# Performance work log

Measured on AMD Instinct MI355X. Metric: run time of the kernel, lower is better.

## Reference

```python
import math
import jax, jax.numpy as jnp
import numpy as np


def _sinkhorn_attn(q, n):
    """Log-domain Sinkhorn-Knopp, eps=1, max_iter=1, uniform marginals.
    cost C = -q @ q^T, so M = (-C + u + v)/eps = S + u + v with S = q q^T.
    Returns transport plan pi = exp(S + u_i + v_j).  q: [B, n, d]."""
    S = jnp.einsum('bnd,bmd->bnm', q, q)            # [B, n, n]
    log_marg = -math.log(n)                          # log(1/n)
    u = log_marg - jax.nn.logsumexp(S, axis=-1)      # [B, n] row update
    v = log_marg - jax.nn.logsumexp(S + u[..., :, None], axis=-2)  # [B, n] col update
    return jnp.exp(S + u[..., :, None] + v[..., None, :])


def reference(x, row_embed, col_embed):
    # x: [B, d, H, W]; row_embed/col_embed: [len_embedding, d//2]
    B, d, H, W = x.shape
    # learned positional embedding: [H, W, d] -> [d, H, W]
    x_emb = col_embed[:W]                             # [W, F]
    y_emb = row_embed[:H]                             # [H, F]
    F = x_emb.shape[-1]
    pos = jnp.concatenate([
        jnp.broadcast_to(x_emb[None, :, :], (H, W, F)),
        jnp.broadcast_to(y_emb[:, None, :], (H, W, F)),
    ], axis=-1).transpose(2, 0, 1)                    # [d, H, W]
    x = x + pos[None]

    n = H * W
    xf = x.reshape(B, d, n).transpose(0, 2, 1)        # [B, n, d] = q = k = v (v unscaled)
    inv_sqrtV = 1.0 / math.sqrt(math.sqrt(d))         # d**-0.25 applied to q and k each
    attn = _sinkhorn_attn(xf * inv_sqrtV, n)          # [B, n, n]
    out = jnp.einsum('bnm,bmd->bnd', attn, xf)        # [B, n, d]
    return out.transpose(0, 2, 1).reshape(B, d, H, W)


def setup_inputs() -> dict:
    key = jax.random.key(0)
    k1, k2, k3 = jax.random.split(key, 3)
    B, d, H, W = 32, 512, 32, 32
    len_emb, F = 32, d // 2
    return {
        'x': jax.random.normal(k1, (B, d, H, W), dtype=jnp.float32),
        'row_embed': jax.random.uniform(k2, (len_emb, F), dtype=jnp.float32),
        'col_embed': jax.random.uniform(k3, (len_emb, F), dtype=jnp.float32),
    }
```

## Files before the change

kernel.cpp:

```cpp
#include <hip/hip_runtime.h>
#include <hip/hip_fp16.h>
#include <math.h>

typedef _Float16 f16;
typedef _Float16 f16x8 __attribute__((ext_vector_type(8)));
typedef _Float16 f16x4 __attribute__((ext_vector_type(4)));
typedef float f32x4 __attribute__((ext_vector_type(4)));

namespace {
constexpr int kB = 32, kD = 512, kN = 1024, kF = 256;
constexpr float kScale = 0.04419417382415922f;
constexpr float kLogMarg = -6.931471805599453f;
constexpr float kMarg = 1.f / 1024.f;
constexpr float kPScale = 16384.f;
constexpr float kPInv = 1.f / 16384.f;
}

__device__ __forceinline__ void gload16(const void* g, void* l) {
  __builtin_amdgcn_global_load_lds(
      (const __attribute__((address_space(1))) void*)g,
      (__attribute__((address_space(3))) void*)l, 16, 0, 0);
}

__global__ __launch_bounds__(256) void k_prep(
    const float* __restrict__ x, const float* __restrict__ re,
    const float* __restrict__ ce, f16* __restrict__ xf,
    f16* __restrict__ xfT, int b0) {
  __shared__ f16 T[64][68];
  const int lb = blockIdx.z;
  const int i0 = blockIdx.x * 64, c0 = blockIdx.y * 64;
  const int t = threadIdx.x;
  const int il = (t & 15) * 4;
  const int cl = t >> 4;
  const size_t xbase = ((size_t)(b0 + lb) * kD) * kN;
#pragma unroll
  for (int p = 0; p < 4; p++) {
    const int c = c0 + cl + 16 * p;
    const int i = i0 + il;
    const float4 xv = *(const float4*)(x + xbase + (size_t)c * kN + i);
    float4 pv;
    if (c < kF) {
      pv.x = ce[((i + 0) & 31) * kF + c];
      pv.y = ce[((i + 1) & 31) * kF + c];
      pv.z = ce[((i + 2) & 31) * kF + c];
      pv.w = ce[((i + 3) & 31) * kF + c];
    } else {
      const float r = re[(i >> 5) * kF + (c - kF)];
      pv.x = r; pv.y = r; pv.z = r; pv.w = r;
    }
    const f16 h0 = (f16)(xv.x + pv.x), h1 = (f16)(xv.y + pv.y);
    const f16 h2 = (f16)(xv.z + pv.z), h3 = (f16)(xv.w + pv.w);
    f16* dT = xfT + ((size_t)lb * kD + c) * kN + i;
    *(f16x4*)dT = (f16x4){h0, h1, h2, h3};
    T[cl + 16 * p][il + 0] = h0; T[cl + 16 * p][il + 1] = h1;
    T[cl + 16 * p][il + 2] = h2; T[cl + 16 * p][il + 3] = h3;
  }
  __syncthreads();
#pragma unroll
  for (int p = 0; p < 4; p++) {
    const int ir = cl + 16 * p;
    const int cc = il;
    const f16 h0 = T[cc + 0][ir], h1 = T[cc + 1][ir];
    const f16 h2 = T[cc + 2][ir], h3 = T[cc + 3][ir];
    f16* dF = xf + ((size_t)lb * kN + i0 + ir) * kD + c0 + cc;
    *(f16x4*)dF = (f16x4){h0, h1, h2, h3};
  }
}

__global__ __launch_bounds__(256) void k_gemm_s(
    const f16* __restrict__ xf, f16* __restrict__ S16,
    float* __restrict__ rp) {
  __shared__ char sm[65536];
  const int nwg = (int)(gridDim.x * gridDim.y * gridDim.z);
  const int lin = (int)(blockIdx.x +
                        gridDim.x * (blockIdx.y + gridDim.y * blockIdx.z));
  const int wid = (lin & 7) * (nwg >> 3) + (lin >> 3);
  const int bx = wid & 7, by = (wid >> 3) & 7, bz = wid >> 6;

  const int lb = bz;
  const int i0 = by * 128, j0 = bx * 128;
  const char* base = (const char*)(xf + (size_t)lb * kN * kD);
  const int t = threadIdx.x;
  const int w = t >> 6, lane = t & 63;
  const int m_off = (w >> 1) * 64, n_off = (w & 1) * 64;
  const int quad = lane >> 4, l15 = lane & 15;
  const int swz = (l15 & 7) << 4;

  int srcA[4], srcB[4], ldsw[4];
#pragma unroll
  for (int p = 0; p < 4; p++) {
    const int off = p * 4096 + w * 1024 + lane * 16;
    const int r = off >> 7;
    const int cb = (off & 127) ^ ((r & 7) << 4);
    srcA[p] = (i0 + r) * (kD * 2) + cb;
    srcB[p] = (j0 + r) * (kD * 2) + cb;
    ldsw[p] = p * 4096 + w * 1024;
  }

  f32x4 acc[4][4];
#pragma unroll
  for (int a = 0; a < 4; a++)
#pragma unroll
    for (int b = 0; b < 4; b++) acc[a][b] = (f32x4){0.f, 0.f, 0.f, 0.f};

#pragma unroll
  for (int p = 0; p < 4; p++) gload16(base + srcA[p], sm + ldsw[p]);
#pragma unroll
  for (int p = 0; p < 4; p++) gload16(base + srcB[p], sm + 16384 + ldsw[p]);
  __syncthreads();

#pragma unroll
  for (int tt = 0; tt < 8; tt++) {
    const int cur = tt & 1, nxt = cur ^ 1;
    if (tt + 1 < 8) {
      const int k0b = (tt + 1) * 128;
#pragma unroll
      for (int p = 0; p < 4; p++)
        gload16(base + srcA[p] + k0b, sm + (nxt << 15) + ldsw[p]);
#pragma unroll
      for (int p = 0; p < 4; p++)
        gload16(base + srcB[p] + k0b, sm + (nxt << 15) + 16384 + ldsw[p]);
    }
    const char* bA = sm + (cur << 15);
    const char* bB = bA + 16384;
#pragma unroll
    for (int kk = 0; kk < 2; kk++) {
      f16x8 af[4], bf[4];
#pragma unroll
      for (int q = 0; q < 4; q++)
        af[q] = *(const f16x8*)(bA + (m_off + 16 * q + l15) * 128 +
                                ((kk * 64 + quad * 16) ^ swz));
#pragma unroll
      for (int q = 0; q < 4; q++)
        bf[q] = *(const f16x8*)(bB + (n_off + 16 * q + l15) * 128 +
                                ((kk * 64 + quad * 16) ^ swz));
#pragma unroll
      for (int qa = 0; qa < 4; qa++)
#pragma unroll
        for (int qb = 0; qb < 4; qb++)
          acc[qa][qb] = __builtin_amdgcn_mfma_f32_16x16x32_f16(
              af[qa], bf[qb], acc[qa][qb], 0, 0, 0);
    }
    __syncthreads();
  }

  f16* Sb = S16 + (size_t)lb * kN * kN;
  const int jt2 = bx * 2 + (w & 1);
  float* rpb = rp + ((size_t)lb * 16 + jt2) * kN + i0 + m_off;
#pragma unroll
  for (int qa = 0; qa < 4; qa++) {
    const int i = i0 + m_off + 16 * qa + quad * 4;
    float rs[4] = {0.f, 0.f, 0.f, 0.f};
#pragma unroll
    for (int qb = 0; qb < 4; qb++) {
      const int j = j0 + n_off + 16 * qb + l15;
#pragma unroll
      for (int r = 0; r < 4; r++) {
        const f16 h = (f16)(acc[qa][qb][r] * kScale);
        Sb[(size_t)(i + r) * kN + j] = h;
        rs[r] += __expf((float)h);
      }
    }
#pragma unroll
    for (int r = 0; r < 4; r++) {
      float s = rs[r];
      s += __shfl_xor(s, 1);
      s += __shfl_xor(s, 2);
      s += __shfl_xor(s, 4);
      s += __shfl_xor(s, 8);
      if (l15 == 0) rpb[16 * qa + 4 * quad + r] = s;
    }
  }
}

__global__ __launch_bounds__(256) void k_u(
    const float* __restrict__ rp, float* __restrict__ u) {
  const int lb = blockIdx.y;
  const int i = blockIdx.x * 256 + threadIdx.x;
  const float* r = rp + (size_t)lb * 16 * kN + i;
  float s = 0.f;
#pragma unroll
  for (int t = 0; t < 16; t++) s += r[(size_t)t * kN];
  u[lb * kN + i] = kLogMarg - __logf(s);
}

__global__ __launch_bounds__(256) void k_cs(
    const f16* __restrict__ S16, const float* __restrict__ u,
    float* __restrict__ cp) {
  const int lb = blockIdx.z;
  const int seg = blockIdx.y;
  const int j = blockIdx.x * 256 + threadIdx.x;
  const f16* Sb = S16 + (size_t)lb * kN * kN + j;
  const float* ub = u + lb * kN + seg * 64;
  const size_t rbase = (size_t)(seg * 64) * kN;
  float s = 0.f;
#pragma unroll 4
  for (int r = 0; r < 64; r++)
    s += __expf((float)Sb[rbase + (size_t)r * kN] + ub[r]);
  cp[((size_t)lb * 16 + seg) * kN + j] = s;
}

__global__ __launch_bounds__(256) void k_v(
    const float* __restrict__ cp, float* __restrict__ ev) {
  const int lb = blockIdx.y;
  const int j = blockIdx.x * 256 + threadIdx.x;
  const float* c = cp + (size_t)lb * 16 * kN + j;
  float s = 0.f;
#pragma unroll
  for (int r = 0; r < 16; r++) s += c[(size_t)r * kN];
  ev[lb * kN + j] = kMarg / s;
}

__global__ __launch_bounds__(256) void k_pt(
    const f16* __restrict__ S16, const float* __restrict__ u,
    const float* __restrict__ ev, f16* __restrict__ t16) {
  const int row = blockIdx.x;
  const float ui = u[row];
  const f16* Sr = S16 + (size_t)row * kN;
  const float* evb = ev + (size_t)(row >> 10) * kN;
  f16* Tr = t16 + (size_t)row * kN;
  const int j = threadIdx.x * 4;
  const f16x4 s = *(const f16x4*)(Sr + j);
  const float4 e = *(const float4*)(evb + j);
  f16x4 o;
  o[0] = (f16)(__expf((float)s[0] + ui) * e.x * kPScale);
  o[1] = (f16)(__expf((float)s[1] + ui) * e.y * kPScale);
  o[2] = (f16)(__expf((float)s[2] + ui) * e.z * kPScale);
  o[3] = (f16)(__expf((float)s[3] + ui) * e.w * kPScale);
  *(f16x4*)(Tr + j) = o;
}

__global__ __launch_bounds__(256) void k_gemm_o(
    const f16* __restrict__ xfT, const f16* __restrict__ P,
    float* __restrict__ out, int b0) {
  __shared__ char sm[65536];
  const int nwg = (int)(gridDim.x * gridDim.y * gridDim.z);
  const int lin = (int)(blockIdx.x +
                        gridDim.x * (blockIdx.y + gridDim.y * blockIdx.z));
  const int wid = (lin & 7) * (nwg >> 3) + (lin >> 3);
  const int bx = wid & 7, by = (wid >> 3) & 3, bz = wid >> 5;

  const int lb = bz;
  const int i0 = bx * 128, c0 = by * 128;
  const char* Ab = (const char*)(xfT + (size_t)lb * kD * kN);
  const char* Bb = (const char*)(P + (size_t)lb * kN * kN);
  const int t = threadIdx.x;
  const int w = t >> 6, lane = t & 63;
  const int m_off = (w >> 1) * 64, n_off = (w & 1) * 64;
  const int quad = lane >> 4, l15 = lane & 15;
  const int swz = (l15 & 7) << 4;

  int srcA[4], srcB[4], ldsw[4];
#pragma unroll
  for (int p = 0; p < 4; p++) {
    const int off = p * 4096 + w * 1024 + lane * 16;
    const int r = off >> 7;
    const int cb = (off & 127) ^ ((r & 7) << 4);
    srcA[p] = (c0 + r) * (kN * 2) + cb;
    srcB[p] = (i0 + r) * (kN * 2) + cb;
    ldsw[p] = p * 4096 + w * 1024;
  }

  f32x4 acc[4][4];
#pragma unroll
  for (int a = 0; a < 4; a++)
#pragma unroll
    for (int b = 0; b < 4; b++) acc[a][b] = (f32x4){0.f, 0.f, 0.f, 0.f};

#pragma unroll
  for (int p = 0; p < 4; p++) gload16(Ab + srcA[p], sm + ldsw[p]);
#pragma unroll
  for (int p = 0; p < 4; p++) gload16(Bb + srcB[p], sm + 16384 + ldsw[p]);
  __syncthreads();

#pragma unroll
  for (int tt = 0; tt < 16; tt++) {
    const int cur = tt & 1, nxt = cur ^ 1;
    if (tt + 1 < 16) {
      const int k0b = (tt + 1) * 128;
#pragma unroll
      for (int p = 0; p < 4; p++)
        gload16(Ab + srcA[p] + k0b, sm + (nxt << 15) + ldsw[p]);
#pragma unroll
      for (int p = 0; p < 4; p++)
        gload16(Bb + srcB[p] + k0b, sm + (nxt << 15) + 16384 + ldsw[p]);
    }
    const char* bA = sm + (cur << 15);
    const char* bB = bA + 16384;
#pragma unroll
    for (int kk = 0; kk < 2; kk++) {
      f16x8 af[4], bf[4];
#pragma unroll
      for (int q = 0; q < 4; q++)
        af[q] = *(const f16x8*)(bA + (m_off + 16 * q + l15) * 128 +
                                ((kk * 64 + quad * 16) ^ swz));
#pragma unroll
      for (int q = 0; q < 4; q++)
        bf[q] = *(const f16x8*)(bB + (n_off + 16 * q + l15) * 128 +
                                ((kk * 64 + quad * 16) ^ swz));
#pragma unroll
      for (int qa = 0; qa < 4; qa++)
#pragma unroll
        for (int qb = 0; qb < 4; qb++)
          acc[qa][qb] = __builtin_amdgcn_mfma_f32_16x16x32_f16(
              af[qa], bf[qb], acc[qa][qb], 0, 0, 0);
    }
    __syncthreads();
  }

  float* ob = out + ((size_t)(b0 + lb) * kD) * kN;
#pragma unroll
  for (int qa = 0; qa < 4; qa++) {
    const int c = c0 + m_off + 16 * qa + quad * 4;
#pragma unroll
    for (int qb = 0; qb < 4; qb++) {
      const int i = i0 + n_off + 16 * qb + l15;
#pragma unroll
      for (int r = 0; r < 4; r++)
        ob[(size_t)(c + r) * kN + i] = acc[qa][qb][r] * kPInv;
    }
  }
}

extern "C" void kernel_launch(void* const* d_in, const int* in_sizes, int n_in,
                              void* d_out, int out_size, void* d_ws, size_t ws_size,
                              hipStream_t stream) {
  const float* x = (const float*)d_in[0];
  const float* re = (const float*)d_in[1];
  const float* ce = (const float*)d_in[2];
  float* out = (float*)d_out;

  char* wsb = (char*)d_ws;
  const size_t perb = 2097152ull + 1048576 + 1048576 + 2097152 +
                      4096 + 4096 + 65536 + 65536;
  int G = (int)(ws_size / perb);
  if (G >= 32) G = 32;
  else if (G >= 16) G = 16;
  else if (G >= 8) G = 8;
  else if (G >= 4) G = 4;
  else if (G < 1) G = 1;
  f16* S16 = (f16*)wsb;
  f16* xf = (f16*)(wsb + (size_t)G * 2097152);
  f16* xfT = (f16*)((char*)xf + (size_t)G * 1048576);
  f16* t16 = (f16*)((char*)xfT + (size_t)G * 1048576);
  float* u = (float*)((char*)t16 + (size_t)G * 2097152);
  float* ev = u + (size_t)G * kN;
  float* rp = ev + (size_t)G * kN;
  float* cp = rp + (size_t)G * 16 * kN;

  for (int b0 = 0; b0 < kB; b0 += G) {
    const int g = (kB - b0 < G) ? (kB - b0) : G;
    k_prep<<<dim3(16, 8, g), 256, 0, stream>>>(x, re, ce, xf, xfT, b0);
    k_gemm_s<<<dim3(8, 8, g), 256, 0, stream>>>(xf, S16, rp);
    k_u<<<dim3(4, g), 256, 0, stream>>>(rp, u);
    k_cs<<<dim3(4, 16, g), 256, 0, stream>>>(S16, u, cp);
    k_v<<<dim3(4, g), 256, 0, stream>>>(cp, ev);
    k_pt<<<g * kN, 256, 0, stream>>>(S16, u, ev, t16);
    k_gemm_o<<<dim3(8, 4, g), 256, 0, stream>>>(xfT, t16, out, b0);
  }
}
```

Measured before the change: 256.1 us.

## Fuse exp-plan materialization into column-sum pass and fold column scaling into output GEMM

```diff
diff --git a/kernel.cpp b/kernel.cpp
--- a/kernel.cpp
+++ b/kernel.cpp
@@ -67,46 +67,47 @@
   }
 }
 
-__global__ __launch_bounds__(256) void k_gemm_s(
+__global__ __launch_bounds__(512) void k_gemm_s(
     const f16* __restrict__ xf, f16* __restrict__ S16,
     float* __restrict__ rp) {
-  __shared__ char sm[65536];
+  __shared__ char sm[131072];
   const int nwg = (int)(gridDim.x * gridDim.y * gridDim.z);
   const int lin = (int)(blockIdx.x +
                         gridDim.x * (blockIdx.y + gridDim.y * blockIdx.z));
   const int wid = (lin & 7) * (nwg >> 3) + (lin >> 3);
-  const int bx = wid & 7, by = (wid >> 3) & 7, bz = wid >> 6;
+  const int bx = wid & 3, by = (wid >> 2) & 3, bz = wid >> 4;
 
   const int lb = bz;
-  const int i0 = by * 128, j0 = bx * 128;
+  const int i0 = by * 256, j0 = bx * 256;
   const char* base = (const char*)(xf + (size_t)lb * kN * kD);
   const int t = threadIdx.x;
   const int w = t >> 6, lane = t & 63;
-  const int m_off = (w >> 1) * 64, n_off = (w & 1) * 64;
+  const int wm = w >> 2, wn = w & 3;
+  const int m_off = wm * 128, n_off = wn * 64;
   const int quad = lane >> 4, l15 = lane & 15;
   const int swz = (l15 & 7) << 4;
 
   int srcA[4], srcB[4], ldsw[4];
 #pragma unroll
   for (int p = 0; p < 4; p++) {
-    const int off = p * 4096 + w * 1024 + lane * 16;
+    const int off = p * 8192 + t * 16;
     const int r = off >> 7;
     const int cb = (off & 127) ^ ((r & 7) << 4);
     srcA[p] = (i0 + r) * (kD * 2) + cb;
     srcB[p] = (j0 + r) * (kD * 2) + cb;
-    ldsw[p] = p * 4096 + w * 1024;
-  }
-
-  f32x4 acc[4][4];
-#pragma unroll
-  for (int a = 0; a < 4; a++)
+    ldsw[p] = p * 8192 + w * 1024;
+  }
+
+  f32x4 acc[8][4];
+#pragma unroll
+  for (int a = 0; a < 8; a++)
 #pragma unroll
     for (int b = 0; b < 4; b++) acc[a][b] = (f32x4){0.f, 0.f, 0.f, 0.f};
 
 #pragma unroll
   for (int p = 0; p < 4; p++) gload16(base + srcA[p], sm + ldsw[p]);
 #pragma unroll
-  for (int p = 0; p < 4; p++) gload16(base + srcB[p], sm + 16384 + ldsw[p]);
+  for (int p = 0; p < 4; p++) gload16(base + srcB[p], sm + 32768 + ldsw[p]);
   __syncthreads();
 
 #pragma unroll
@@ -116,18 +117,18 @@
       const int k0b = (tt + 1) * 128;
 #pragma unroll
       for (int p = 0; p < 4; p++)
-        gload16(base + srcA[p] + k0b, sm + (nxt << 15) + ldsw[p]);
+        gload16(base + srcA[p] + k0b, sm + (nxt << 16) + ldsw[p]);
 #pragma unroll
       for (int p = 0; p < 4; p++)
-        gload16(base + srcB[p] + k0b, sm + (nxt << 15) + 16384 + ldsw[p]);
-    }
-    const char* bA = sm + (cur << 15);
-    const char* bB = bA + 16384;
+        gload16(base + srcB[p] + k0b, sm + (nxt << 16) + 32768 + ldsw[p]);
+    }
+    const char* bA = sm + (cur << 16);
+    const char* bB = bA + 32768;
 #pragma unroll
     for (int kk = 0; kk < 2; kk++) {
-      f16x8 af[4], bf[4];
-#pragma unroll
-      for (int q = 0; q < 4; q++)
+      f16x8 af[8], bf[4];
+#pragma unroll
+      for (int q = 0; q < 8; q++)
         af[q] = *(const f16x8*)(bA + (m_off + 16 * q + l15) * 128 +
                                 ((kk * 64 + quad * 16) ^ swz));
 #pragma unroll
@@ -135,7 +136,7 @@
         bf[q] = *(const f16x8*)(bB + (n_off + 16 * q + l15) * 128 +
                                 ((kk * 64 + quad * 16) ^ swz));
 #pragma unroll
-      for (int qa = 0; qa < 4; qa++)
+      for (int qa = 0; qa < 8; qa++)
 #pragma unroll
         for (int qb = 0; qb < 4; qb++)
           acc[qa][qb] = __builtin_amdgcn_mfma_f32_16x16x32_f16(
@@ -145,10 +146,10 @@
   }
 
   f16* Sb = S16 + (size_t)lb * kN * kN;
-  const int jt2 = bx * 2 + (w & 1);
-  float* rpb = rp + ((size_t)lb * 16 + jt2) * kN + i0 + m_off;
-#pragma unroll
-  for (int qa = 0; qa < 4; qa++) {
+  const int jt = bx * 4 + wn;
+  float* rpb = rp + ((size_t)lb * 16 + jt) * kN + i0 + m_off;
+#pragma unroll
+  for (int qa = 0; qa < 8; qa++) {
     const int i = i0 + m_off + 16 * qa + quad * 4;
     float rs[4] = {0.f, 0.f, 0.f, 0.f};
 #pragma unroll
@@ -186,17 +187,21 @@
 
 __global__ __launch_bounds__(256) void k_cs(
     const f16* __restrict__ S16, const float* __restrict__ u,
-    float* __restrict__ cp) {
+    float* __restrict__ cp, f16* __restrict__ E16) {
   const int lb = blockIdx.z;
   const int seg = blockIdx.y;
   const int j = blockIdx.x * 256 + threadIdx.x;
   const f16* Sb = S16 + (size_t)lb * kN * kN + j;
+  f16* Eb = E16 + (size_t)lb * kN * kN + j;
   const float* ub = u + lb * kN + seg * 64;
   const size_t rbase = (size_t)(seg * 64) * kN;
   float s = 0.f;
 #pragma unroll 4
-  for (int r = 0; r < 64; r++)
-    s += __expf((float)Sb[rbase + (size_t)r * kN] + ub[r]);
+  for (int r = 0; r < 64; r++) {
+    const float eS = __expf((float)Sb[rbase + (size_t)r * kN] + ub[r]);
+    s += eS;
+    Eb[rbase + (size_t)r * kN] = (f16)(eS * kPScale);
+  }
   cp[((size_t)lb * 16 + seg) * kN + j] = s;
 }
 
@@ -211,87 +216,97 @@
   ev[lb * kN + j] = kMarg / s;
 }
 
-__global__ __launch_bounds__(256) void k_pt(
-    const f16* __restrict__ S16, const float* __restrict__ u,
-    const float* __restrict__ ev, f16* __restrict__ t16) {
-  const int row = blockIdx.x;
-  const float ui = u[row];
-  const f16* Sr = S16 + (size_t)row * kN;
-  const float* evb = ev + (size_t)(row >> 10) * kN;
-  f16* Tr = t16 + (size_t)row * kN;
-  const int j = threadIdx.x * 4;
-  const f16x4 s = *(const f16x4*)(Sr + j);
-  const float4 e = *(const float4*)(evb + j);
-  f16x4 o;
-  o[0] = (f16)(__expf((float)s[0] + ui) * e.x * kPScale);
-  o[1] = (f16)(__expf((float)s[1] + ui) * e.y * kPScale);
-  o[2] = (f16)(__expf((float)s[2] + ui) * e.z * kPScale);
-  o[3] = (f16)(__expf((float)s[3] + ui) * e.w * kPScale);
-  *(f16x4*)(Tr + j) = o;
-}
-
-__global__ __launch_bounds__(256) void k_gemm_o(
-    const f16* __restrict__ xfT, const f16* __restrict__ P,
-    float* __restrict__ out, int b0) {
-  __shared__ char sm[65536];
+__global__ __launch_bounds__(512) void k_gemm_o(
+    const f16* __restrict__ xfT, const f16* __restrict__ E16,
+    const float* __restrict__ ev, float* __restrict__ out, int b0) {
+  __shared__ char sm[131072];
   const int nwg = (int)(gridDim.x * gridDim.y * gridDim.z);
   const int lin = (int)(blockIdx.x +
                         gridDim.x * (blockIdx.y + gridDim.y * blockIdx.z));
   const int wid = (lin & 7) * (nwg >> 3) + (lin >> 3);
-  const int bx = wid & 7, by = (wid >> 3) & 3, bz = wid >> 5;
+  const int bx = wid & 3, by = (wid >> 2) & 1, bz = wid >> 3;
 
   const int lb = bz;
-  const int i0 = bx * 128, c0 = by * 128;
+  const int i0 = bx * 256, c0 = by * 256;
   const char* Ab = (const char*)(xfT + (size_t)lb * kD * kN);
-  const char* Bb = (const char*)(P + (size_t)lb * kN * kN);
+  const char* Bb = (const char*)(E16 + (size_t)lb * kN * kN);
+  const float* evb = ev + (size_t)lb * kN;
   const int t = threadIdx.x;
   const int w = t >> 6, lane = t & 63;
-  const int m_off = (w >> 1) * 64, n_off = (w & 1) * 64;
+  const int wm = w >> 2, wn = w & 3;
+  const int m_off = wm * 128, n_off = wn * 64;
   const int quad = lane >> 4, l15 = lane & 15;
   const int swz = (l15 & 7) << 4;
 
-  int srcA[4], srcB[4], ldsw[4];
-#pragma unroll
-  for (int p = 0; p < 4; p++) {
-    const int off = p * 4096 + w * 1024 + lane * 16;
+  int srcAlin[4], dstA[4], srcB[4], ldsw[4], evcol[4];
+#pragma unroll
+  for (int p = 0; p < 4; p++) {
+    const int off = p * 8192 + t * 16;
     const int r = off >> 7;
-    const int cb = (off & 127) ^ ((r & 7) << 4);
-    srcA[p] = (c0 + r) * (kN * 2) + cb;
+    const int cbl = off & 127;
+    const int cb = cbl ^ ((r & 7) << 4);
+    srcAlin[p] = (c0 + r) * (kN * 2) + cbl;
+    dstA[p] = r * 128 + cb;
     srcB[p] = (i0 + r) * (kN * 2) + cb;
-    ldsw[p] = p * 4096 + w * 1024;
-  }
-
-  f32x4 acc[4][4];
-#pragma unroll
-  for (int a = 0; a < 4; a++)
+    ldsw[p] = p * 8192 + w * 1024;
+    evcol[p] = cbl >> 1;
+  }
+
+  f32x4 acc[8][4];
+#pragma unroll
+  for (int a = 0; a < 8; a++)
 #pragma unroll
     for (int b = 0; b < 4; b++) acc[a][b] = (f32x4){0.f, 0.f, 0.f, 0.f};
 
-#pragma unroll
-  for (int p = 0; p < 4; p++) gload16(Ab + srcA[p], sm + ldsw[p]);
-#pragma unroll
-  for (int p = 0; p < 4; p++) gload16(Bb + srcB[p], sm + 16384 + ldsw[p]);
+  f16x8 al[4];
+  float4 e0[4], e1[4];
+#pragma unroll
+  for (int p = 0; p < 4; p++) {
+    al[p] = *(const f16x8*)(Ab + srcAlin[p]);
+    e0[p] = *(const float4*)(evb + evcol[p]);
+    e1[p] = *(const float4*)(evb + evcol[p] + 4);
+  }
+#pragma unroll
+  for (int p = 0; p < 4; p++) gload16(Bb + srcB[p], sm + 32768 + ldsw[p]);
+#pragma unroll
+  for (int p = 0; p < 4; p++) {
+    f16x8 pr;
+    pr[0] = (f16)((float)al[p][0] * e0[p].x);
+    pr[1] = (f16)((float)al[p][1] * e0[p].y);
+    pr[2] = (f16)((float)al[p][2] * e0[p].z);
+    pr[3] = (f16)((float)al[p][3] * e0[p].w);
+    pr[4] = (f16)((float)al[p][4] * e1[p].x);
+    pr[5] = (f16)((float)al[p][5] * e1[p].y);
+    pr[6] = (f16)((float)al[p][6] * e1[p].z);
+    pr[7] = (f16)((float)al[p][7] * e1[p].w);
+    *(f16x8*)(sm + dstA[p]) = pr;
+  }
   __syncthreads();
 
 #pragma unroll
   for (int tt = 0; tt < 16; tt++) {
     const int cur = tt & 1, nxt = cur ^ 1;
-    if (tt + 1 < 16) {
+    const bool pf = (tt + 1 < 16);
+    if (pf) {
       const int k0b = (tt + 1) * 128;
+      const int k0f = (tt + 1) * 64;
+#pragma unroll
+      for (int p = 0; p < 4; p++) {
+        al[p] = *(const f16x8*)(Ab + srcAlin[p] + k0b);
+        e0[p] = *(const float4*)(evb + k0f + evcol[p]);
+        e1[p] = *(const float4*)(evb + k0f + evcol[p] + 4);
+      }
 #pragma unroll
       for (int p = 0; p < 4; p++)
-        gload16(Ab + srcA[p] + k0b, sm + (nxt << 15) + ldsw[p]);
-#pragma unroll
-      for (int p = 0; p < 4; p++)
-        gload16(Bb + srcB[p] + k0b, sm + (nxt << 15) + 16384 + ldsw[p]);
-    }
-    const char* bA = sm + (cur << 15);
-    const char* bB = bA + 16384;
+        gload16(Bb + srcB[p] + k0b, sm + (nxt << 16) + 32768 + ldsw[p]);
+    }
+    const char* bA = sm + (cur << 16);
+    const char* bB = bA + 32768;
 #pragma unroll
     for (int kk = 0; kk < 2; kk++) {
-      f16x8 af[4], bf[4];
-#pragma unroll
-      for (int q = 0; q < 4; q++)
+      f16x8 af[8], bf[4];
+#pragma unroll
+      for (int q = 0; q < 8; q++)
         af[q] = *(const f16x8*)(bA + (m_off + 16 * q + l15) * 128 +
                                 ((kk * 64 + quad * 16) ^ swz));
 #pragma unroll
@@ -299,18 +314,33 @@
         bf[q] = *(const f16x8*)(bB + (n_off + 16 * q + l15) * 128 +
                                 ((kk * 64 + quad * 16) ^ swz));
 #pragma unroll
-      for (int qa = 0; qa < 4; qa++)
+      for (int qa = 0; qa < 8; qa++)
 #pragma unroll
         for (int qb = 0; qb < 4; qb++)
           acc[qa][qb] = __builtin_amdgcn_mfma_f32_16x16x32_f16(
               af[qa], bf[qb], acc[qa][qb], 0, 0, 0);
     }
+    if (pf) {
+#pragma unroll
+      for (int p = 0; p < 4; p++) {
+        f16x8 pr;
+        pr[0] = (f16)((float)al[p][0] * e0[p].x);
+        pr[1] = (f16)((float)al[p][1] * e0[p].y);
+        pr[2] = (f16)((float)al[p][2] * e0[p].z);
+        pr[3] = (f16)((float)al[p][3] * e0[p].w);
+        pr[4] = (f16)((float)al[p][4] * e1[p].x);
+        pr[5] = (f16)((float)al[p][5] * e1[p].y);
+        pr[6] = (f16)((float)al[p][6] * e1[p].z);
+        pr[7] = (f16)((float)al[p][7] * e1[p].w);
+        *(f16x8*)(sm + (nxt << 16) + dstA[p]) = pr;
+      }
+    }
     __syncthreads();
   }
 
   float* ob = out + ((size_t)(b0 + lb) * kD) * kN;
 #pragma unroll
-  for (int qa = 0; qa < 4; qa++) {
+  for (int qa = 0; qa < 8; qa++) {
     const int c = c0 + m_off + 16 * qa + quad * 4;
 #pragma unroll
     for (int qb = 0; qb < 4; qb++) {
@@ -342,8 +372,8 @@
   f16* S16 = (f16*)wsb;
   f16* xf = (f16*)(wsb + (size_t)G * 2097152);
   f16* xfT = (f16*)((char*)xf + (size_t)G * 1048576);
-  f16* t16 = (f16*)((char*)xfT + (size_t)G * 1048576);
-  float* u = (float*)((char*)t16 + (size_t)G * 2097152);
+  f16* E16 = (f16*)((char*)xfT + (size_t)G * 1048576);
+  float* u = (float*)((char*)E16 + (size_t)G * 2097152);
   float* ev = u + (size_t)G * kN;
   float* rp = ev + (size_t)G * kN;
   float* cp = rp + (size_t)G * 16 * kN;
@@ -351,11 +381,10 @@
   for (int b0 = 0; b0 < kB; b0 += G) {
     const int g = (kB - b0 < G) ? (kB - b0) : G;
     k_prep<<<dim3(16, 8, g), 256, 0, stream>>>(x, re, ce, xf, xfT, b0);
-    k_gemm_s<<<dim3(8, 8, g), 256, 0, stream>>>(xf, S16, rp);
+    k_gemm_s<<<dim3(4, 4, g), 512, 0, stream>>>(xf, S16, rp);
     k_u<<<dim3(4, g), 256, 0, stream>>>(rp, u);
-    k_cs<<<dim3(4, 16, g), 256, 0, stream>>>(S16, u, cp);
+    k_cs<<<dim3(4, 16, g), 256, 0, stream>>>(S16, u, cp, E16);
     k_v<<<dim3(4, g), 256, 0, stream>>>(cp, ev);
-    k_pt<<<g * kN, 256, 0, stream>>>(S16, u, ev, t16);
-    k_gemm_o<<<dim3(8, 4, g), 256, 0, stream>>>(xfT, t16, out, b0);
-  }
-}
+    k_gemm_o<<<dim3(4, 2, g), 512, 0, stream>>>(xfT, E16, ev, out, b0);
+  }
+}
```

After: 257.0 us. No clear change (+0.3%).

## Fuse transport-plan exponentiation into output GEMM with larger tiles and staged pipeline

Applied to the files above, without the earlier changes.

```diff
diff --git a/kernel.cpp b/kernel.cpp
--- a/kernel.cpp
+++ b/kernel.cpp
@@ -11,8 +11,6 @@
 constexpr int kB = 32, kD = 512, kN = 1024, kF = 256;
 constexpr float kScale = 0.04419417382415922f;
 constexpr float kLogMarg = -6.931471805599453f;
-constexpr float kMarg = 1.f / 1024.f;
-constexpr float kPScale = 16384.f;
 constexpr float kPInv = 1.f / 16384.f;
 }
 
@@ -189,128 +187,192 @@
     float* __restrict__ cp) {
   const int lb = blockIdx.z;
   const int seg = blockIdx.y;
-  const int j = blockIdx.x * 256 + threadIdx.x;
-  const f16* Sb = S16 + (size_t)lb * kN * kN + j;
+  const int j = threadIdx.x * 4;
+  const f16* Sb = S16 + (size_t)lb * kN * kN + (size_t)(seg * 64) * kN + j;
   const float* ub = u + lb * kN + seg * 64;
-  const size_t rbase = (size_t)(seg * 64) * kN;
-  float s = 0.f;
-#pragma unroll 4
-  for (int r = 0; r < 64; r++)
-    s += __expf((float)Sb[rbase + (size_t)r * kN] + ub[r]);
-  cp[((size_t)lb * 16 + seg) * kN + j] = s;
+  float s0 = 0.f, s1 = 0.f, s2 = 0.f, s3 = 0.f;
+#pragma unroll 8
+  for (int r = 0; r < 64; r++) {
+    const f16x4 v = *(const f16x4*)(Sb + (size_t)r * kN);
+    const float ur = ub[r];
+    s0 += __expf((float)v[0] + ur);
+    s1 += __expf((float)v[1] + ur);
+    s2 += __expf((float)v[2] + ur);
+    s3 += __expf((float)v[3] + ur);
+  }
+  float4 o = {s0, s1, s2, s3};
+  *(float4*)(cp + ((size_t)lb * 16 + seg) * kN + j) = o;
 }
 
 __global__ __launch_bounds__(256) void k_v(
-    const float* __restrict__ cp, float* __restrict__ ev) {
+    const float* __restrict__ cp, float* __restrict__ evp) {
   const int lb = blockIdx.y;
   const int j = blockIdx.x * 256 + threadIdx.x;
   const float* c = cp + (size_t)lb * 16 * kN + j;
   float s = 0.f;
 #pragma unroll
   for (int r = 0; r < 16; r++) s += c[(size_t)r * kN];
-  ev[lb * kN + j] = kMarg / s;
-}
-
-__global__ __launch_bounds__(256) void k_pt(
-    const f16* __restrict__ S16, const float* __restrict__ u,
-    const float* __restrict__ ev, f16* __restrict__ t16) {
-  const int row = blockIdx.x;
-  const float ui = u[row];
-  const f16* Sr = S16 + (size_t)row * kN;
-  const float* evb = ev + (size_t)(row >> 10) * kN;
-  f16* Tr = t16 + (size_t)row * kN;
-  const int j = threadIdx.x * 4;
-  const f16x4 s = *(const f16x4*)(Sr + j);
-  const float4 e = *(const float4*)(evb + j);
-  f16x4 o;
-  o[0] = (f16)(__expf((float)s[0] + ui) * e.x * kPScale);
-  o[1] = (f16)(__expf((float)s[1] + ui) * e.y * kPScale);
-  o[2] = (f16)(__expf((float)s[2] + ui) * e.z * kPScale);
-  o[3] = (f16)(__expf((float)s[3] + ui) * e.w * kPScale);
-  *(f16x4*)(Tr + j) = o;
-}
-
-__global__ __launch_bounds__(256) void k_gemm_o(
-    const f16* __restrict__ xfT, const f16* __restrict__ P,
+  evp[lb * kN + j] = 16.f / s;
+}
+
+#define AF_READ(q)                                                          \
+  _Pragma("unroll")                                                         \
+  for (int pa = 0; pa < 2; pa++)                                            \
+    _Pragma("unroll")                                                       \
+    for (int kk = 0; kk < 2; kk++)                                          \
+      af[pa][kk] = *(const f16x8*)(bA + (m_off + 32*(q) + 16*pa + l15)*128  \
+                                   + ((kk*64 + quad*16) ^ swz));
+
+#define MFMA_PH(q)                                                          \
+  __builtin_amdgcn_s_setprio(1);                                            \
+  _Pragma("unroll")                                                         \
+  for (int pa = 0; pa < 2; pa++)                                            \
+    _Pragma("unroll")                                                       \
+    for (int qb = 0; qb < 4; qb++)                                          \
+      _Pragma("unroll")                                                     \
+      for (int kk = 0; kk < 2; kk++)                                        \
+        acc[2*(q)+pa][qb] = __builtin_amdgcn_mfma_f32_16x16x32_f16(         \
+            af[pa][kk], bf[qb][kk], acc[2*(q)+pa][qb], 0, 0, 0);            \
+  __builtin_amdgcn_s_setprio(0);
+
+__global__ __launch_bounds__(512) void k_gemm_o(
+    const f16* __restrict__ xfT, const f16* __restrict__ S16,
+    const float* __restrict__ u, const float* __restrict__ evp,
     float* __restrict__ out, int b0) {
-  __shared__ char sm[65536];
+  __shared__ char sm[135168];
   const int nwg = (int)(gridDim.x * gridDim.y * gridDim.z);
   const int lin = (int)(blockIdx.x +
                         gridDim.x * (blockIdx.y + gridDim.y * blockIdx.z));
   const int wid = (lin & 7) * (nwg >> 3) + (lin >> 3);
-  const int bx = wid & 7, by = (wid >> 3) & 3, bz = wid >> 5;
+  const int bx = wid & 3, by = (wid >> 2) & 1, bz = wid >> 3;
 
   const int lb = bz;
-  const int i0 = bx * 128, c0 = by * 128;
+  const int i0 = bx * 256, c0 = by * 256;
   const char* Ab = (const char*)(xfT + (size_t)lb * kD * kN);
-  const char* Bb = (const char*)(P + (size_t)lb * kN * kN);
+  const char* Bb = (const char*)(S16 + (size_t)lb * kN * kN);
   const int t = threadIdx.x;
   const int w = t >> 6, lane = t & 63;
-  const int m_off = (w >> 1) * 64, n_off = (w & 1) * 64;
+  const int wm = w >> 2, wn = w & 3;
+  const int m_off = wm * 128, n_off = wn * 64;
   const int quad = lane >> 4, l15 = lane & 15;
   const int swz = (l15 & 7) << 4;
 
   int srcA[4], srcB[4], ldsw[4];
 #pragma unroll
   for (int p = 0; p < 4; p++) {
-    const int off = p * 4096 + w * 1024 + lane * 16;
+    const int off = p * 8192 + t * 16;
     const int r = off >> 7;
     const int cb = (off & 127) ^ ((r & 7) << 4);
     srcA[p] = (c0 + r) * (kN * 2) + cb;
     srcB[p] = (i0 + r) * (kN * 2) + cb;
-    ldsw[p] = p * 4096 + w * 1024;
-  }
-
-  f32x4 acc[4][4];
-#pragma unroll
-  for (int a = 0; a < 4; a++)
+    ldsw[p] = p * 8192 + w * 1024;
+  }
+
+  float* evl = (float*)(sm + 131072);
+  *(float2*)(evl + t * 2) = *(const float2*)(evp + (size_t)lb * kN + t * 2);
+  float u4[4];
+  const float* ub = u + (size_t)lb * kN + i0 + n_off + l15;
+#pragma unroll
+  for (int qb = 0; qb < 4; qb++) u4[qb] = ub[16 * qb];
+  asm volatile("s_waitcnt vmcnt(0) lgkmcnt(0)" ::: "memory");
+  __builtin_amdgcn_sched_barrier(0);
+
+#pragma unroll
+  for (int p = 0; p < 4; p++) gload16(Bb + srcB[p], sm + 65536 + ldsw[p]);
+  gload16(Ab + srcA[0], sm + ldsw[0]);
+  gload16(Ab + srcA[2], sm + ldsw[2]);
+  gload16(Ab + srcA[1], sm + ldsw[1]);
+  gload16(Ab + srcA[3], sm + ldsw[3]);
+#pragma unroll
+  for (int p = 0; p < 4; p++)
+    gload16(Bb + srcB[p] + 128, sm + 65536 + 32768 + ldsw[p]);
+  f32x4 acc[8][4];
+#pragma unroll
+  for (int a = 0; a < 8; a++)
 #pragma unroll
     for (int b = 0; b < 4; b++) acc[a][b] = (f32x4){0.f, 0.f, 0.f, 0.f};
-
-#pragma unroll
-  for (int p = 0; p < 4; p++) gload16(Ab + srcA[p], sm + ldsw[p]);
-#pragma unroll
-  for (int p = 0; p < 4; p++) gload16(Bb + srcB[p], sm + 16384 + ldsw[p]);
-  __syncthreads();
+  asm volatile("s_waitcnt vmcnt(6)" ::: "memory");
+  __builtin_amdgcn_s_barrier();
+  __builtin_amdgcn_sched_barrier(0);
 
 #pragma unroll
   for (int tt = 0; tt < 16; tt++) {
     const int cur = tt & 1, nxt = cur ^ 1;
+    const char* bA = sm + cur * 32768;
+    const char* bB = sm + 65536 + cur * 32768;
+    char* wA = sm + nxt * 32768;
+    char* wB = sm + 65536 + cur * 32768;
+    const int kA = (tt + 1) * 128, kBB = (tt + 2) * 128;
+    f16x8 bf[4][2], af[2][2];
+    f16x8 raw[4][2];
+#pragma unroll
+    for (int qb = 0; qb < 4; qb++)
+#pragma unroll
+      for (int kk = 0; kk < 2; kk++)
+        raw[qb][kk] = *(const f16x8*)(bB + (n_off + 16 * qb + l15) * 128 +
+                                      ((kk * 64 + quad * 16) ^ swz));
+    AF_READ(0)
+    float4 e0[2], e1[2];
+#pragma unroll
+    for (int kk = 0; kk < 2; kk++) {
+      const float* ep = evl + tt * 64 + kk * 32 + quad * 8;
+      e0[kk] = *(const float4*)ep;
+      e1[kk] = *(const float4*)(ep + 4);
+    }
+    asm volatile("s_waitcnt lgkmcnt(0)" ::: "memory");
+    __builtin_amdgcn_sched_barrier(0);
+    __builtin_amdgcn_s_barrier();
+#pragma unroll
+    for (int qb = 0; qb < 4; qb++)
+#pragma unroll
+      for (int kk = 0; kk < 2; kk++) {
+        f16x8 o;
+        o[0] = (f16)(__expf((float)raw[qb][kk][0] + u4[qb]) * e0[kk].x);
+        o[1] = (f16)(__expf((float)raw[qb][kk][1] + u4[qb]) * e0[kk].y);
+        o[2] = (f16)(__expf((float)raw[qb][kk][2] + u4[qb]) * e0[kk].z);
+        o[3] = (f16)(__expf((float)raw[qb][kk][3] + u4[qb]) * e0[kk].w);
+        o[4] = (f16)(__expf((float)raw[qb][kk][4] + u4[qb]) * e1[kk].x);
+        o[5] = (f16)(__expf((float)raw[qb][kk][5] + u4[qb]) * e1[kk].y);
+        o[6] = (f16)(__expf((float)raw[qb][kk][6] + u4[qb]) * e1[kk].z);
+        o[7] = (f16)(__expf((float)raw[qb][kk][7] + u4[qb]) * e1[kk].w);
+        bf[qb][kk] = o;
+      }
+    MFMA_PH(0)
     if (tt + 1 < 16) {
-      const int k0b = (tt + 1) * 128;
+      gload16(Ab + srcA[0] + kA, wA + ldsw[0]);
+      gload16(Ab + srcA[2] + kA, wA + ldsw[2]);
+    }
+    AF_READ(1)
+    __builtin_amdgcn_s_barrier();
+    MFMA_PH(1)
+    if (tt == 15) { asm volatile("s_waitcnt vmcnt(0)" ::: "memory"); }
+    else          { asm volatile("s_waitcnt vmcnt(6)" ::: "memory"); }
+    __builtin_amdgcn_s_barrier();
+    __builtin_amdgcn_sched_barrier(0);
+    AF_READ(2)
+    __builtin_amdgcn_s_barrier();
+    MFMA_PH(2)
+    if (tt + 1 < 16) {
+      gload16(Ab + srcA[1] + kA, wA + ldsw[1]);
+      gload16(Ab + srcA[3] + kA, wA + ldsw[3]);
+    }
+    if (tt + 2 < 16) {
 #pragma unroll
       for (int p = 0; p < 4; p++)
-        gload16(Ab + srcA[p] + k0b, sm + (nxt << 15) + ldsw[p]);
-#pragma unroll
-      for (int p = 0; p < 4; p++)
-        gload16(Bb + srcB[p] + k0b, sm + (nxt << 15) + 16384 + ldsw[p]);
-    }
-    const char* bA = sm + (cur << 15);
-    const char* bB = bA + 16384;
-#pragma unroll
-    for (int kk = 0; kk < 2; kk++) {
-      f16x8 af[4], bf[4];
-#pragma unroll
-      for (int q = 0; q < 4; q++)
-        af[q] = *(const f16x8*)(bA + (m_off + 16 * q + l15) * 128 +
-                                ((kk * 64 + quad * 16) ^ swz));
-#pragma unroll
-      for (int q = 0; q < 4; q++)
-        bf[q] = *(const f16x8*)(bB + (n_off + 16 * q + l15) * 128 +
-                                ((kk * 64 + quad * 16) ^ swz));
-#pragma unroll
-      for (int qa = 0; qa < 4; qa++)
-#pragma unroll
-        for (int qb = 0; qb < 4; qb++)
-          acc[qa][qb] = __builtin_amdgcn_mfma_f32_16x16x32_f16(
-              af[qa], bf[qb], acc[qa][qb], 0, 0, 0);
-    }
-    __syncthreads();
+        gload16(Bb + srcB[p] + kBB, wB + ldsw[p]);
+    }
+    AF_READ(3)
+    __builtin_amdgcn_s_barrier();
+    MFMA_PH(3)
+    if (tt + 2 < 16)      { asm volatile("s_waitcnt vmcnt(6)" ::: "memory"); }
+    else if (tt + 1 < 16) { asm volatile("s_waitcnt vmcnt(2)" ::: "memory"); }
+    __builtin_amdgcn_s_barrier();
+    __builtin_amdgcn_sched_barrier(0);
   }
 
   float* ob = out + ((size_t)(b0 + lb) * kD) * kN;
 #pragma unroll
-  for (int qa = 0; qa < 4; qa++) {
+  for (int qa = 0; qa < 8; qa++) {
     const int c = c0 + m_off + 16 * qa + quad * 4;
 #pragma unroll
     for (int qb = 0; qb < 4; qb++) {
@@ -331,8 +393,8 @@
   float* out = (float*)d_out;
 
   char* wsb = (char*)d_ws;
-  const size_t perb = 2097152ull + 1048576 + 1048576 + 2097152 +
-                      4096 + 4096 + 65536 + 65536;
+  const size_t perb = 2097152ull + 1048576 + 1048576 + 4096 + 4096 +
+                      65536 + 65536;
   int G = (int)(ws_size / perb);
   if (G >= 32) G = 32;
   else if (G >= 16) G = 16;
@@ -342,10 +404,9 @@
   f16* S16 = (f16*)wsb;
   f16* xf = (f16*)(wsb + (size_t)G * 2097152);
   f16* xfT = (f16*)((char*)xf + (size_t)G * 1048576);
-  f16* t16 = (f16*)((char*)xfT + (size_t)G * 1048576);
-  float* u = (float*)((char*)t16 + (size_t)G * 2097152);
-  float* ev = u + (size_t)G * kN;
-  float* rp = ev + (size_t)G * kN;
+  float* u = (float*)((char*)xfT + (size_t)G * 1048576);
+  float* evp = u + (size_t)G * kN;
+  float* rp = evp + (size_t)G * kN;
   float* cp = rp + (size_t)G * 16 * kN;
 
   for (int b0 = 0; b0 < kB; b0 += G) {
@@ -353,9 +414,8 @@
     k_prep<<<dim3(16, 8, g), 256, 0, stream>>>(x, re, ce, xf, xfT, b0);
     k_gemm_s<<<dim3(8, 8, g), 256, 0, stream>>>(xf, S16, rp);
     k_u<<<dim3(4, g), 256, 0, stream>>>(rp, u);
-    k_cs<<<dim3(4, 16, g), 256, 0, stream>>>(S16, u, cp);
-    k_v<<<dim3(4, g), 256, 0, stream>>>(cp, ev);
-    k_pt<<<g * kN, 256, 0, stream>>>(S16, u, ev, t16);
-    k_gemm_o<<<dim3(8, 4, g), 256, 0, stream>>>(xfT, t16, out, b0);
-  }
-}
+    k_cs<<<dim3(1, 16, g), 256, 0, stream>>>(S16, u, cp);
+    k_v<<<dim3(4, g), 256, 0, stream>>>(cp, evp);
+    k_gemm_o<<<dim3(4, 2, g), 512, 0, stream>>>(xfT, S16, u, evp, out, b0);
+  }
+}
```

Result: no change. 257.9 us (+0.7%).
